# Kernel tuning notes

Hardware: AMD Instinct MI355X
Metric: run time of the kernel (lower is better)

## Reference

```python
import jax, jax.numpy as jnp
import numpy as np

V, BS, E, H, L, FC = 50257, 1024, 768, 12, 6, 4
B, T = 4, 1024
HS = E // H
FF = FC * E
EPS = 1e-5


def setup_inputs() -> dict:
    key = jax.random.key(0)
    ks = jax.random.split(key, 24)
    s = 0.02
    inp = {
        'idx': jax.random.randint(ks[0], (B, T), 0, V),
        'targets': jax.random.randint(ks[1], (B, T), 0, V),
        'tok_emb': jax.random.normal(ks[2], (V, E), jnp.float32) * s,
        'pos_emb': jax.random.normal(ks[3], (BS, E), jnp.float32) * s,
        'Wq': jax.random.normal(ks[4], (L, H, E, HS), jnp.float32) * s,
        'Wk': jax.random.normal(ks[5], (L, H, E, HS), jnp.float32) * s,
        'Wv': jax.random.normal(ks[6], (L, H, E, HS), jnp.float32) * s,
        'Wo': jax.random.normal(ks[7], (L, E, E), jnp.float32) * s,
        'bo': jnp.zeros((L, E), jnp.float32),
        'ln1_s': jnp.ones((L, E), jnp.float32),
        'ln1_b': jnp.zeros((L, E), jnp.float32),
        'ln2_s': jnp.ones((L, E), jnp.float32),
        'ln2_b': jnp.zeros((L, E), jnp.float32),
        'W1': jax.random.normal(ks[8], (L, E, FF), jnp.float32) * s,
        'b1': jnp.zeros((L, FF), jnp.float32),
        'W2': jax.random.normal(ks[9], (L, FF, E), jnp.float32) * s,
        'b2': jnp.zeros((L, E), jnp.float32),
        'lnf_s': jnp.ones((E,), jnp.float32),
        'lnf_b': jnp.zeros((E,), jnp.float32),
        'Wlm': jax.random.normal(ks[10], (E, V), jnp.float32) * s,
        'blm': jnp.zeros((V,), jnp.float32),
    }
    return inp


def _ln(x, scale, bias):
    mu = x.mean(-1, keepdims=True)
    var = ((x - mu) ** 2).mean(-1, keepdims=True)
    return (x - mu) * jax.lax.rsqrt(var + EPS) * scale + bias


def _forward(idx, targets, tok_emb, pos_emb, Wq, Wk, Wv, Wo, bo,
             ln1_s, ln1_b, ln2_s, ln2_b, W1, b1, W2, b2,
             lnf_s, lnf_b, Wlm, blm):
    Bc, Tc = idx.shape
    x = tok_emb[idx] + pos_emb[:Tc]                      # [B,T,E]
    causal = jnp.tril(jnp.ones((Tc, Tc), bool))          # [T,T]

    def block(x, p):
        wq, wk, wv, wo_, bo_, l1s, l1b, l2s, l2b, w1, b1_, w2, b2_ = p
        h = _ln(x, l1s, l1b)
        q = jnp.einsum('bte,hed->bhtd', h, wq)
        k = jnp.einsum('bte,hed->bhtd', h, wk)
        v = jnp.einsum('bte,hed->bhtd', h, wv)
        scores = jnp.einsum('bhtd,bhsd->bhts', q, k) * (HS ** -0.5)
        scores = jnp.where(causal, scores, -jnp.inf)
        att = jax.nn.softmax(scores, axis=-1)            # [B,H,T,T]
        o = jnp.einsum('bhts,bhsd->bhtd', att, v)
        o = o.transpose(0, 2, 1, 3).reshape(Bc, Tc, E)   # concat heads
        x = x + jnp.einsum('bte,ef->btf', o, wo_) + bo_
        h2 = _ln(x, l2s, l2b)
        f = jax.nn.relu(jnp.einsum('bte,ef->btf', h2, w1) + b1_)
        x = x + jnp.einsum('btf,fe->bte', f, w2) + b2_
        return x, None

    layers = (Wq, Wk, Wv, Wo, bo, ln1_s, ln1_b, ln2_s, ln2_b, W1, b1, W2, b2)
    x, _ = jax.lax.scan(block, x, layers)
    x = _ln(x, lnf_s, lnf_b)
    logits = jnp.einsum('bte,ev->btv', x, Wlm) + blm     # [B,T,V]
    logp = jax.nn.log_softmax(logits, axis=-1)
    nll = -jnp.take_along_axis(logp, targets[..., None], axis=-1)[..., 0]
    loss = nll.mean()
    return logits, loss


def reference(idx, targets, tok_emb, pos_emb, Wq, Wk, Wv, Wo, bo,
              ln1_s, ln1_b, ln2_s, ln2_b, W1, b1, W2, b2,
              lnf_s, lnf_b, Wlm, blm):
    return _forward(idx, targets, tok_emb, pos_emb, Wq, Wk, Wv, Wo, bo,
                    ln1_s, ln1_b, ln2_s, ln2_b, W1, b1, W2, b2,
                    lnf_s, lnf_b, Wlm, blm)
```

## Files before the change

kernel.cpp:

```cpp
#include <hip/hip_runtime.h>
#include <hip/hip_bf16.h>
#include <cstdint>
#include <cstddef>

#define NB 4
#define NT 1024
#define NE 768
#define NH 12
#define NHS 64
#define NL 6
#define NFF 3072
#define NV 50257
#define NVP 50304
#define NTOK (NB*NT)
#define NCB_LM (NVP/128)
#define QKVS 2304

typedef __attribute__((ext_vector_type(8))) short short8;
typedef __attribute__((ext_vector_type(4))) float f32x4;
typedef __hip_bfloat16 bf16;

__global__ __launch_bounds__(256) void embed_kernel(
    const int* __restrict__ idx, const float* __restrict__ tok,
    const float* __restrict__ pos, float* __restrict__ x)
{
  int bt = blockIdx.x;
  int token = idx[bt];
  int t = bt & (NT - 1);
  const float* tr = tok + (size_t)token * NE;
  const float* pr = pos + (size_t)t * NE;
  float* xr = x + (size_t)bt * NE;
  for (int i = threadIdx.x; i < NE; i += 256)
    xr[i] = tr[i] + pr[i];
}

__global__ __launch_bounds__(256) void ln_kernel(
    const float* __restrict__ in, const float* __restrict__ sc,
    const float* __restrict__ bi, bf16* __restrict__ out)
{
  int row = blockIdx.x, tid = threadIdx.x;
  const float* xr = in + (size_t)row * NE;
  float v0 = xr[tid], v1 = xr[tid + 256], v2 = xr[tid + 512];
  float s = v0 + v1 + v2;
  float ss = v0 * v0 + v1 * v1 + v2 * v2;
  #pragma unroll
  for (int o = 32; o > 0; o >>= 1) {
    s  += __shfl_xor(s, o);
    ss += __shfl_xor(ss, o);
  }
  __shared__ float r1[4], r2[4];
  if ((tid & 63) == 0) { r1[tid >> 6] = s; r2[tid >> 6] = ss; }
  __syncthreads();
  float tot = r1[0] + r1[1] + r1[2] + r1[3];
  float tss = r2[0] + r2[1] + r2[2] + r2[3];
  float mu  = tot * (1.f / NE);
  float var = tss * (1.f / NE) - mu * mu;
  float rs  = rsqrtf(var + 1e-5f);
  bf16* orow = out + (size_t)row * NE;
  orow[tid]       = __float2bfloat16((v0 - mu) * rs * sc[tid]       + bi[tid]);
  orow[tid + 256] = __float2bfloat16((v1 - mu) * rs * sc[tid + 256] + bi[tid + 256]);
  orow[tid + 512] = __float2bfloat16((v2 - mu) * rs * sc[tid + 512] + bi[tid + 512]);
}

__global__ __launch_bounds__(256) void tconv_kernel(
    const float* __restrict__ src, bf16* __restrict__ dst,
    int R, int Cs, int Cd)
{
  __shared__ float t[32][33];
  int z = blockIdx.z;
  src += (size_t)z * R * Cs;
  dst += (size_t)z * Cd * R;
  int c0 = blockIdx.x * 32, r0 = blockIdx.y * 32;
  int tx = threadIdx.x & 31, ty = threadIdx.x >> 5;
  #pragma unroll
  for (int i = 0; i < 32; i += 8) {
    int r = r0 + ty + i, c = c0 + tx;
    t[ty + i][tx] = (c < Cs) ? src[(size_t)r * Cs + c] : 0.f;
  }
  __syncthreads();
  #pragma unroll
  for (int i = 0; i < 32; i += 8) {
    int c = c0 + ty + i, r = r0 + tx;
    if (c < Cd) dst[(size_t)c * R + r] = __float2bfloat16(t[tx][ty + i]);
  }
}

template<int MREP, bool NTST>
__global__ __launch_bounds__(256) void gemm_bf(
    const bf16* __restrict__ A,
    const bf16* __restrict__ BT,
    float* __restrict__ Cf, bf16* __restrict__ Cbf,
    const float* __restrict__ bias, const float* __restrict__ Rres,
    float* __restrict__ ps,
    int M, int N, int K, int relu, int ncb)
{
  constexpr int BMT = MREP * 32;
  __shared__ bf16 As[BMT][64];
  __shared__ bf16 Bs[128][64];
  __shared__ float ps2[BMT][2];
  int tid = threadIdx.x;
  int lane = tid & 63;
  int w = __builtin_amdgcn_readfirstlane(tid >> 6);
  int wr = w >> 1, wc = w & 1;
  int row0 = blockIdx.y * BMT;
  int col0 = blockIdx.x * 128;

  f32x4 acc[MREP][4] = {};

  for (int k0 = 0; k0 < K; k0 += 64) {
    #pragma unroll
    for (int r = 0; r < MREP; ++r) {
      int c = r * 256 + tid;
      int trow = c >> 3;
      int schunk = (c & 7) ^ (trow & 7);
      const bf16* ga = A + (size_t)(row0 + trow) * K + k0 + (schunk << 3);
      __builtin_amdgcn_global_load_lds(
          (const __attribute__((address_space(1))) void*)ga,
          (__attribute__((address_space(3))) void*)((char*)&As[0][0] + (unsigned)c * 16),
          16, 0, 0);
    }
    #pragma unroll
    for (int r = 0; r < 4; ++r) {
      int c = r * 256 + tid;
      int trow = c >> 3;
      int schunk = (c & 7) ^ (trow & 7);
      const bf16* gb = BT + (size_t)(col0 + trow) * K + k0 + (schunk << 3);
      __builtin_amdgcn_global_load_lds(
          (const __attribute__((address_space(1))) void*)gb,
          (__attribute__((address_space(3))) void*)((char*)&Bs[0][0] + (unsigned)c * 16),
          16, 0, 0);
    }
    __syncthreads();
    int l15 = lane & 15;
    int g8 = (lane >> 4) << 3;
    int sx = (l15 & 7) << 3;
    #pragma unroll
    for (int kk = 0; kk < 64; kk += 32) {
      short8 a[MREP], b[4];
      #pragma unroll
      for (int m = 0; m < MREP; ++m)
        a[m] = *(const short8*)&As[wr * (MREP * 16) + m * 16 + l15][(kk + g8) ^ sx];
      #pragma unroll
      for (int n = 0; n < 4; ++n)
        b[n] = *(const short8*)&Bs[wc * 64 + n * 16 + l15][(kk + g8) ^ sx];
      #pragma unroll
      for (int m = 0; m < MREP; ++m)
        #pragma unroll
        for (int n = 0; n < 4; ++n)
          acc[m][n] = __builtin_amdgcn_mfma_f32_16x16x32_bf16(a[m], b[n], acc[m][n], 0, 0, 0);
    }
    __syncthreads();
  }

  int cr = lane >> 4;
  int cc = lane & 15;
  #pragma unroll
  for (int m = 0; m < MREP; ++m) {
    #pragma unroll
    for (int n = 0; n < 4; ++n) {
      int col = col0 + wc * 64 + n * 16 + cc;
      if (col >= N) continue;
      float bv = bias ? bias[col] : 0.f;
      #pragma unroll
      for (int e = 0; e < 4; ++e) {
        int row = row0 + wr * (MREP * 16) + m * 16 + cr * 4 + e;
        float v = acc[m][n][e] + bv;
        size_t off = (size_t)row * N + col;
        if (Rres) v += Rres[off];
        if (relu) v = fmaxf(v, 0.f);
        if (Cf) {
          if (NTST) __builtin_nontemporal_store(v, &Cf[off]);
          else      Cf[off] = v;
        }
        if (Cbf) Cbf[off] = __float2bfloat16(v);
      }
    }
  }

  if (ps) {
    #pragma unroll
    for (int m = 0; m < MREP; ++m) {
      #pragma unroll
      for (int e = 0; e < 4; ++e) {
        float ssum = 0.f;
        #pragma unroll
        for (int n = 0; n < 4; ++n) {
          int col = col0 + wc * 64 + n * 16 + cc;
          float val = (col < N) ? (acc[m][n][e] + (bias ? bias[col] : 0.f)) : -1e30f;
          ssum += __expf(val);
        }
        ssum += __shfl_xor(ssum, 1);
        ssum += __shfl_xor(ssum, 2);
        ssum += __shfl_xor(ssum, 4);
        ssum += __shfl_xor(ssum, 8);
        if (cc == 0) {
          int rl = wr * (MREP * 16) + m * 16 + cr * 4 + e;
          ps2[rl][wc] = ssum;
        }
      }
    }
    __syncthreads();
    for (int i = tid; i < BMT; i += 256) {
      size_t o = (size_t)(row0 + i) * ncb + blockIdx.x;
      ps[o] = ps2[i][0] + ps2[i][1];
    }
  }
}

static __device__ inline unsigned short bfbits(float x) {
  bf16 h = __float2bfloat16(x);
  return *reinterpret_cast<unsigned short*>(&h);
}

__global__ __launch_bounds__(256) void fattn_kernel(
    const bf16* __restrict__ QKV, bf16* __restrict__ O)
{
  __shared__ unsigned short Ks[64][72];
  __shared__ unsigned short Vt[64][72];
  __shared__ unsigned short Pl[4][16][72];
  int qt = blockIdx.x, h = blockIdx.y, b = blockIdx.z;
  int tid = threadIdx.x;
  int lane = tid & 63;
  int w = tid >> 6;
  int l15 = lane & 15, g = lane >> 4;
  int brow = b * NT;
  int qbase = qt * 64;
  int q_loc = w * 16 + l15;

  short8 bq[2];
  {
    const bf16* qp = QKV + (size_t)(brow + qbase + q_loc) * QKVS + h * 64 + g * 8;
    bq[0] = *(const short8*)qp;
    bq[1] = *(const short8*)(qp + 32);
  }

  float m_run = -1e30f, l_run = 0.f;
  f32x4 acc[4] = {};

  for (int kt = 0; kt <= qt; ++kt) {
    int s0 = kt * 64;
    #pragma unroll
    for (int i = 0; i < 2; ++i) {
      int c = tid + i * 256;
      int row = c >> 3, colg = (c & 7) * 8;
      const bf16* kp = QKV + (size_t)(brow + s0 + row) * QKVS + NE + h * 64 + colg;
      const bf16* vp = QKV + (size_t)(brow + s0 + row) * QKVS + 2 * NE + h * 64 + colg;
      short8 kv = *(const short8*)kp;
      short8 vv = *(const short8*)vp;
      *(short8*)&Ks[row][colg] = kv;
      #pragma unroll
      for (int j = 0; j < 8; ++j)
        Vt[colg + j][row] = (unsigned short)vv[j];
    }
    __syncthreads();

    f32x4 sf[4] = {};
    #pragma unroll
    for (int kk = 0; kk < 2; ++kk) {
      #pragma unroll
      for (int m = 0; m < 4; ++m) {
        short8 a = *(const short8*)&Ks[m * 16 + l15][kk * 32 + g * 8];
        sf[m] = __builtin_amdgcn_mfma_f32_16x16x32_bf16(a, bq[kk], sf[m], 0, 0, 0);
      }
    }

    float sv[4][4];
    float mx = -1e30f;
    bool diag = (kt == qt);
    #pragma unroll
    for (int m = 0; m < 4; ++m)
      #pragma unroll
      for (int e = 0; e < 4; ++e) {
        float v = sf[m][e] * 0.125f;
        if (diag) {
          int sl = m * 16 + g * 4 + e;
          if (sl > q_loc) v = -1e30f;
        }
        sv[m][e] = v;
        mx = fmaxf(mx, v);
      }
    mx = fmaxf(mx, __shfl_xor(mx, 16));
    mx = fmaxf(mx, __shfl_xor(mx, 32));
    float m_new = fmaxf(m_run, mx);
    float p[4][4];
    float rs = 0.f;
    #pragma unroll
    for (int m = 0; m < 4; ++m)
      #pragma unroll
      for (int e = 0; e < 4; ++e) {
        float pe = __expf(sv[m][e] - m_new);
        p[m][e] = pe;
        rs += pe;
      }
    rs += __shfl_xor(rs, 16);
    rs += __shfl_xor(rs, 32);
    float sc_old = __expf(m_run - m_new);
    l_run = l_run * sc_old + rs;
    m_run = m_new;
    #pragma unroll
    for (int dm = 0; dm < 4; ++dm)
      #pragma unroll
      for (int e = 0; e < 4; ++e)
        acc[dm][e] *= sc_old;

    #pragma unroll
    for (int m = 0; m < 4; ++m)
      #pragma unroll
      for (int ep = 0; ep < 2; ++ep) {
        unsigned u = (unsigned)bfbits(p[m][2 * ep]) |
                     ((unsigned)bfbits(p[m][2 * ep + 1]) << 16);
        *(unsigned*)&Pl[w][l15][m * 16 + g * 4 + ep * 2] = u;
      }

    #pragma unroll
    for (int ks = 0; ks < 2; ++ks) {
      short8 pb = *(const short8*)&Pl[w][l15][ks * 32 + g * 8];
      #pragma unroll
      for (int dm = 0; dm < 4; ++dm) {
        short8 av = *(const short8*)&Vt[dm * 16 + l15][ks * 32 + g * 8];
        acc[dm] = __builtin_amdgcn_mfma_f32_16x16x32_bf16(av, pb, acc[dm], 0, 0, 0);
      }
    }
    __syncthreads();
  }

  float inv = 1.f / l_run;
  bf16* op = O + (size_t)(brow + qbase + q_loc) * NE + h * 64;
  #pragma unroll
  for (int dm = 0; dm < 4; ++dm)
    #pragma unroll
    for (int ep = 0; ep < 2; ++ep) {
      int d = dm * 16 + g * 4 + ep * 2;
      unsigned u = (unsigned)bfbits(acc[dm][2 * ep] * inv) |
                   ((unsigned)bfbits(acc[dm][2 * ep + 1] * inv) << 16);
      *(unsigned*)((unsigned short*)op + d) = u;
    }
}

__global__ __launch_bounds__(128) void nll_finish(
    const float* __restrict__ ps,
    const float* __restrict__ logits, const int* __restrict__ targets,
    float* __restrict__ nll)
{
  int row = blockIdx.x, tid = threadIdx.x;
  float s = 0.f;
  for (int i = tid; i < NCB_LM; i += 128)
    s += ps[(size_t)row * NCB_LM + i];
  #pragma unroll
  for (int o = 32; o > 0; o >>= 1) s += __shfl_xor(s, o);
  __shared__ float ss[2];
  if ((tid & 63) == 0) ss[tid >> 6] = s;
  __syncthreads();
  if (tid == 0) {
    float S = ss[0] + ss[1];
    float tgt = logits[(size_t)row * NV + targets[row]];
    nll[row] = logf(S) - tgt;
  }
}

__global__ __launch_bounds__(256) void loss_kernel(
    const float* __restrict__ nll, float* __restrict__ out)
{
  int tid = threadIdx.x;
  float s = 0.f;
  for (int i = tid; i < NTOK; i += 256) s += nll[i];
  #pragma unroll
  for (int o = 32; o > 0; o >>= 1) s += __shfl_xor(s, o);
  __shared__ float red[4];
  if ((tid & 63) == 0) red[tid >> 6] = s;
  __syncthreads();
  if (tid == 0) out[0] = (red[0] + red[1] + red[2] + red[3]) * (1.f / NTOK);
}

static inline void gemm(const bf16* A, const bf16* BT,
                        float* Cf, bf16* Cbf,
                        const float* bias, const float* Rres, float* ps,
                        int M, int N, int Npad, int K, int relu,
                        int mrep, bool ntst, hipStream_t st)
{
  int ncb = Npad / 128;
  dim3 g(ncb, M / (mrep * 32));
  if (mrep == 4) {
    if (ntst)
      gemm_bf<4, true><<<g, dim3(256), 0, st>>>(A, BT, Cf, Cbf, bias, Rres, ps, M, N, K, relu, ncb);
    else
      gemm_bf<4, false><<<g, dim3(256), 0, st>>>(A, BT, Cf, Cbf, bias, Rres, ps, M, N, K, relu, ncb);
  } else {
    gemm_bf<2, false><<<g, dim3(256), 0, st>>>(A, BT, Cf, Cbf, bias, Rres, ps, M, N, K, relu, ncb);
  }
}

extern "C" void kernel_launch(void* const* d_in, const int* in_sizes, int n_in,
                              void* d_out, int out_size, void* d_ws, size_t ws_size,
                              hipStream_t stream)
{
  const int*   idx     = (const int*)  d_in[0];
  const int*   targets = (const int*)  d_in[1];
  const float* tok_emb = (const float*)d_in[2];
  const float* pos_emb = (const float*)d_in[3];
  const float* Wq      = (const float*)d_in[4];
  const float* Wk      = (const float*)d_in[5];
  const float* Wv      = (const float*)d_in[6];
  const float* Wo      = (const float*)d_in[7];
  const float* bo      = (const float*)d_in[8];
  const float* ln1_s   = (const float*)d_in[9];
  const float* ln1_b   = (const float*)d_in[10];
  const float* ln2_s   = (const float*)d_in[11];
  const float* ln2_b   = (const float*)d_in[12];
  const float* W1      = (const float*)d_in[13];
  const float* b1      = (const float*)d_in[14];
  const float* W2      = (const float*)d_in[15];
  const float* b2      = (const float*)d_in[16];
  const float* lnf_s   = (const float*)d_in[17];
  const float* lnf_b   = (const float*)d_in[18];
  const float* Wlm     = (const float*)d_in[19];
  const float* blm     = (const float*)d_in[20];
  float* out = (float*)d_out;

  const size_t XE = (size_t)NTOK * NE;
  char* p = (char*)d_ws;
  float* x     = (float*)p;         p += XE * 4;
  bf16* h_bf   = (bf16*)p;          p += XE * 2;
  bf16* qkv_bf = (bf16*)p;          p += (size_t)NTOK * QKVS * 2;
  bf16* att_bf = (bf16*)p;          p += XE * 2;
  bf16* f_bf   = (bf16*)p;          p += (size_t)NTOK * NFF * 2;
  bf16* wqkv   = (bf16*)p;          p += (size_t)QKVS * NE * 2;
  bf16* wto    = (bf16*)p;          p += (size_t)NE * NE * 2;
  bf16* wt1    = (bf16*)p;          p += (size_t)NFF * NE * 2;
  bf16* wt2    = (bf16*)p;          p += (size_t)NE * NFF * 2;
  bf16* wtlm   = (bf16*)p;          p += (size_t)NVP * NE * 2;
  float* psb   = (float*)p;         p += (size_t)NTOK * NCB_LM * 4;
  float* nll   = (float*)p;         p += (size_t)NTOK * 4;

  embed_kernel<<<dim3(NTOK), dim3(256), 0, stream>>>(idx, tok_emb, pos_emb, x);

  for (int l = 0; l < NL; ++l) {
    const float* wq_l = Wq + (size_t)l * NH * NE * NHS;
    const float* wk_l = Wk + (size_t)l * NH * NE * NHS;
    const float* wv_l = Wv + (size_t)l * NH * NE * NHS;
    const float* wo_l = Wo + (size_t)l * NE * NE;
    const float* w1_l = W1 + (size_t)l * NE * NFF;
    const float* w2_l = W2 + (size_t)l * NFF * NE;

    ln_kernel<<<dim3(NTOK), dim3(256), 0, stream>>>(x, ln1_s + l*NE, ln1_b + l*NE, h_bf);

    tconv_kernel<<<dim3(2, 24, NH), dim3(256), 0, stream>>>(wq_l, wqkv, NE, NHS, NHS);
    tconv_kernel<<<dim3(2, 24, NH), dim3(256), 0, stream>>>(wk_l, wqkv + (size_t)NE*NE, NE, NHS, NHS);
    tconv_kernel<<<dim3(2, 24, NH), dim3(256), 0, stream>>>(wv_l, wqkv + (size_t)2*NE*NE, NE, NHS, NHS);
    tconv_kernel<<<dim3(24, 24, 1), dim3(256), 0, stream>>>(wo_l, wto, NE, NE, NE);
    tconv_kernel<<<dim3(96, 24, 1), dim3(256), 0, stream>>>(w1_l, wt1, NE, NFF, NFF);
    tconv_kernel<<<dim3(24, 96, 1), dim3(256), 0, stream>>>(w2_l, wt2, NFF, NE, NE);

    gemm(h_bf, wqkv, nullptr, qkv_bf, nullptr, nullptr, nullptr,
         NTOK, QKVS, QKVS, NE, 0, 4, false, stream);

    fattn_kernel<<<dim3(NT / 64, NH, NB), dim3(256), 0, stream>>>(qkv_bf, att_bf);

    gemm(att_bf, wto, x, nullptr, bo + l*NE, x, nullptr,
         NTOK, NE, NE, NE, 0, 2, false, stream);

    ln_kernel<<<dim3(NTOK), dim3(256), 0, stream>>>(x, ln2_s + l*NE, ln2_b + l*NE, h_bf);

    gemm(h_bf, wt1, nullptr, f_bf, b1 + l*NFF, nullptr, nullptr,
         NTOK, NFF, NFF, NE, 1, 4, false, stream);
    gemm(f_bf, wt2, x, nullptr, b2 + l*NE, x, nullptr,
         NTOK, NE, NE, NFF, 0, 2, false, stream);
  }

  ln_kernel<<<dim3(NTOK), dim3(256), 0, stream>>>(x, lnf_s, lnf_b, h_bf);
  tconv_kernel<<<dim3(NVP/32, 24, 1), dim3(256), 0, stream>>>(Wlm, wtlm, NE, NV, NVP);
  gemm(h_bf, wtlm, out, nullptr, blm, nullptr, psb,
       NTOK, NV, NVP, NE, 0, 4, true, stream);

  nll_finish<<<dim3(NTOK), dim3(128), 0, stream>>>(psb, out, targets, nll);
  loss_kernel<<<dim3(1), dim3(256), 0, stream>>>(nll, out + (size_t)NTOK * NV);
}
```

Measured before the change: 2.380 ms.

## Remap LM-head GEMM blocks into column supergroups and drop swizzle/nontemporal stores

The LM-head GEMM now runs on a 1D grid that groups 8 column blocks into a supergroup iterating over all row tiles, so nearby blocks share the same weight columns in L2. The LDS XOR swizzle is disabled for that launch, and the nontemporal store path for the logits output is removed everywhere. These aim to improve cache reuse of the large vocab weight matrix. The cost is possible LDS bank conflicts without the swizzle and extra cache pollution from the large logits writes.

Measured after the change: 2.447 ms. 1.03x slower.

```diff
diff --git a/kernel.cpp b/kernel.cpp
--- a/kernel.cpp
+++ b/kernel.cpp
@@ -85,7 +85,7 @@
   }
 }
 
-template<int MREP, bool NTST>
+template<int MREP, bool SWZ, bool XMAP>
 __global__ __launch_bounds__(256) void gemm_bf(
     const bf16* __restrict__ A,
     const bf16* __restrict__ BT,
@@ -102,8 +102,19 @@
   int lane = tid & 63;
   int w = __builtin_amdgcn_readfirstlane(tid >> 6);
   int wr = w >> 1, wc = w & 1;
-  int row0 = blockIdx.y * BMT;
-  int col0 = blockIdx.x * 128;
+  int row0, col0, cb;
+  if (XMAP) {
+    int super = blockIdx.x >> 8;
+    int within = blockIdx.x & 255;
+    cb = super * 8 + (within & 7);
+    if (cb >= ncb) return;
+    row0 = (within >> 3) * BMT;
+    col0 = cb * 128;
+  } else {
+    cb = blockIdx.x;
+    row0 = blockIdx.y * BMT;
+    col0 = cb * 128;
+  }
 
   f32x4 acc[MREP][4] = {};
 
@@ -112,7 +123,7 @@
     for (int r = 0; r < MREP; ++r) {
       int c = r * 256 + tid;
       int trow = c >> 3;
-      int schunk = (c & 7) ^ (trow & 7);
+      int schunk = SWZ ? ((c & 7) ^ (trow & 7)) : (c & 7);
       const bf16* ga = A + (size_t)(row0 + trow) * K + k0 + (schunk << 3);
       __builtin_amdgcn_global_load_lds(
           (const __attribute__((address_space(1))) void*)ga,
@@ -123,7 +134,7 @@
     for (int r = 0; r < 4; ++r) {
       int c = r * 256 + tid;
       int trow = c >> 3;
-      int schunk = (c & 7) ^ (trow & 7);
+      int schunk = SWZ ? ((c & 7) ^ (trow & 7)) : (c & 7);
       const bf16* gb = BT + (size_t)(col0 + trow) * K + k0 + (schunk << 3);
       __builtin_amdgcn_global_load_lds(
           (const __attribute__((address_space(1))) void*)gb,
@@ -133,7 +144,7 @@
     __syncthreads();
     int l15 = lane & 15;
     int g8 = (lane >> 4) << 3;
-    int sx = (l15 & 7) << 3;
+    int sx = SWZ ? ((l15 & 7) << 3) : 0;
     #pragma unroll
     for (int kk = 0; kk < 64; kk += 32) {
       short8 a[MREP], b[4];
@@ -168,10 +179,7 @@
         size_t off = (size_t)row * N + col;
         if (Rres) v += Rres[off];
         if (relu) v = fmaxf(v, 0.f);
-        if (Cf) {
-          if (NTST) __builtin_nontemporal_store(v, &Cf[off]);
-          else      Cf[off] = v;
-        }
+        if (Cf)  Cf[off] = v;
         if (Cbf) Cbf[off] = __float2bfloat16(v);
       }
     }
@@ -201,7 +209,7 @@
     }
     __syncthreads();
     for (int i = tid; i < BMT; i += 256) {
-      size_t o = (size_t)(row0 + i) * ncb + blockIdx.x;
+      size_t o = (size_t)(row0 + i) * ncb + cb;
       ps[o] = ps2[i][0] + ps2[i][1];
     }
   }
@@ -376,18 +384,14 @@
                         float* Cf, bf16* Cbf,
                         const float* bias, const float* Rres, float* ps,
                         int M, int N, int Npad, int K, int relu,
-                        int mrep, bool ntst, hipStream_t st)
+                        int mrep, hipStream_t st)
 {
   int ncb = Npad / 128;
   dim3 g(ncb, M / (mrep * 32));
-  if (mrep == 4) {
-    if (ntst)
-      gemm_bf<4, true><<<g, dim3(256), 0, st>>>(A, BT, Cf, Cbf, bias, Rres, ps, M, N, K, relu, ncb);
-    else
-      gemm_bf<4, false><<<g, dim3(256), 0, st>>>(A, BT, Cf, Cbf, bias, Rres, ps, M, N, K, relu, ncb);
-  } else {
-    gemm_bf<2, false><<<g, dim3(256), 0, st>>>(A, BT, Cf, Cbf, bias, Rres, ps, M, N, K, relu, ncb);
-  }
+  if (mrep == 4)
+    gemm_bf<4, true, false><<<g, dim3(256), 0, st>>>(A, BT, Cf, Cbf, bias, Rres, ps, M, N, K, relu, ncb);
+  else
+    gemm_bf<2, true, false><<<g, dim3(256), 0, st>>>(A, BT, Cf, Cbf, bias, Rres, ps, M, N, K, relu, ncb);
 }
 
 extern "C" void kernel_launch(void* const* d_in, const int* in_sizes, int n_in,
@@ -452,25 +456,31 @@
     tconv_kernel<<<dim3(24, 96, 1), dim3(256), 0, stream>>>(w2_l, wt2, NFF, NE, NE);
 
     gemm(h_bf, wqkv, nullptr, qkv_bf, nullptr, nullptr, nullptr,
-         NTOK, QKVS, QKVS, NE, 0, 4, false, stream);
+         NTOK, QKVS, QKVS, NE, 0, 4, stream);
 
     fattn_kernel<<<dim3(NT / 64, NH, NB), dim3(256), 0, stream>>>(qkv_bf, att_bf);
 
     gemm(att_bf, wto, x, nullptr, bo + l*NE, x, nullptr,
-         NTOK, NE, NE, NE, 0, 2, false, stream);
+         NTOK, NE, NE, NE, 0, 2, stream);
 
     ln_kernel<<<dim3(NTOK), dim3(256), 0, stream>>>(x, ln2_s + l*NE, ln2_b + l*NE, h_bf);
 
     gemm(h_bf, wt1, nullptr, f_bf, b1 + l*NFF, nullptr, nullptr,
-         NTOK, NFF, NFF, NE, 1, 4, false, stream);
+         NTOK, NFF, NFF, NE, 1, 4, stream);
     gemm(f_bf, wt2, x, nullptr, b2 + l*NE, x, nullptr,
-         NTOK, NE, NE, NFF, 0, 2, false, stream);
+         NTOK, NE, NE, NFF, 0, 2, stream);
   }
 
   ln_kernel<<<dim3(NTOK), dim3(256), 0, stream>>>(x, lnf_s, lnf_b, h_bf);
   tconv_kernel<<<dim3(NVP/32, 24, 1), dim3(256), 0, stream>>>(Wlm, wtlm, NE, NV, NVP);
-  gemm(h_bf, wtlm, out, nullptr, blm, nullptr, psb,
-       NTOK, NV, NVP, NE, 0, 4, true, stream);
+
+  {
+    int nsuper = (NCB_LM + 7) / 8;
+    dim3 g(nsuper * 256);
+    gemm_bf<4, false, true><<<g, dim3(256), 0, stream>>>(
+        h_bf, wtlm, out, nullptr, blm, nullptr, psb,
+        NTOK, NV, NE, 0, NCB_LM);
+  }
 
   nll_finish<<<dim3(NTOK), dim3(128), 0, stream>>>(psb, out, targets, nll);
   loss_kernel<<<dim3(1), dim3(256), 0, stream>>>(nll, out + (size_t)NTOK * NV);
```
